# Optimization experiments

Hardware: AMD Instinct MI355X
Metric: run time of the kernel (lower is better)

Reference implementation:

```python
import jax, jax.numpy as jnp
import numpy as np

INPUT_DIM = 1024
NUM_OUTPUTS = 1024
BIT_SIZE = 256


def setup_inputs() -> dict:
    key = jax.random.key(0)
    k1, k2 = jax.random.split(key)
    # x: binary input bits, shape (input_dim, bit_size)
    x = jax.random.randint(k1, (INPUT_DIM, BIT_SIZE), 0, 2).astype(jnp.int32)
    # kernel: per-(input, output) Bernoulli probabilities in [0, 1)
    kernel = jax.random.uniform(k2, (INPUT_DIM, NUM_OUTPUTS), dtype=jnp.float32)
    return {"x": x, "kernel": kernel}


def reference(x, kernel):
    # Sample per-weight Bernoulli bit vectors: w[i, n, b] ~ Bernoulli(kernel[i, n])
    # (fused equivalent of the original nested-loop np.random.binomial calls)
    rng = jax.random.key(42)
    u = jax.random.uniform(rng, kernel.shape + (BIT_SIZE,), dtype=kernel.dtype)
    w = u < kernel[:, :, None]  # bool (input_dim, num_outputs, bit_size)

    # Original loop: temp = (x & w[:, n]).sum(axis=0); y[n] = (temp > 0)
    # == OR-reduction over input_dim of the bitwise AND.
    xb = x.astype(bool)  # (input_dim, bit_size)
    y = jnp.any(xb[:, None, :] & w, axis=0)  # (num_outputs, bit_size)
    return y.astype(jnp.float32)
```

## Files before the change

### kernel.cpp

```cpp
#include <hip/hip_runtime.h>


#define INPUT_DIM 1024
#define NUM_OUTPUTS 1024
#define BIT_SIZE 256

__device__ __forceinline__ uint32_t rotl32(uint32_t v, int r) {
    return (v << r) | (v >> (32 - r));
}

__device__ __forceinline__ void threefry2x32(uint32_t k0, uint32_t k1,
                                             uint32_t& x0, uint32_t& x1) {
    const uint32_t ks0 = k0;
    const uint32_t ks1 = k1;
    const uint32_t ks2 = k0 ^ k1 ^ 0x1BD11BDAu;
    x0 += ks0;
    x1 += ks1;
#define TF_ROUND(r) { x0 += x1; x1 = rotl32(x1, (r)); x1 ^= x0; }
    TF_ROUND(13) TF_ROUND(15) TF_ROUND(26) TF_ROUND(6)
    x0 += ks1; x1 += ks2 + 1u;
    TF_ROUND(17) TF_ROUND(29) TF_ROUND(16) TF_ROUND(24)
    x0 += ks2; x1 += ks0 + 2u;
    TF_ROUND(13) TF_ROUND(15) TF_ROUND(26) TF_ROUND(6)
    x0 += ks0; x1 += ks1 + 3u;
    TF_ROUND(17) TF_ROUND(29) TF_ROUND(16) TF_ROUND(24)
    x0 += ks1; x1 += ks2 + 4u;
    TF_ROUND(13) TF_ROUND(15) TF_ROUND(26) TF_ROUND(6)
    x0 += ks2; x1 += ks0 + 5u;
#undef TF_ROUND
}

__global__ __launch_bounds__(256) void BitLayer_25391846654323_kernel(
        const int* __restrict__ x,
        const float* __restrict__ kern,
        float* __restrict__ out) {
    const int tid = threadIdx.x;
    const int b = blockIdx.x >> 2;
    const int n = ((blockIdx.x & 3) << 8) + tid;
    const uint32_t nb = ((uint32_t)n << 8) | (uint32_t)b;
    const int wave = tid >> 6;
    const int lane = tid & 63;

    __shared__ uint32_t smask[32];
#pragma unroll
    for (int k = 0; k < 4; ++k) {
        const int i = (k << 8) + tid;
        const unsigned long long bal = __ballot(x[(i << 8) + b] != 0);
        if ((lane & 31) == 0) {
            smask[(k << 3) + (wave << 1) + (lane >> 5)] =
                (uint32_t)(bal >> (lane & 32));
        }
    }
    __syncthreads();

    uint32_t done = 0;
    for (int w = 0; w < 32; ++w) {
        uint32_t m = smask[w];
        while (m) {
            const int j = __builtin_ctz(m);
            m &= m - 1;
            const int i = (w << 5) + j;
            const float p = kern[(i << 10) + n];
            if (!done) {
                uint32_t c0 = (((uint32_t)(i & 511)) << 18) | nb;
                uint32_t c1 = c0 + (1u << 27);
                threefry2x32(0u, 42u, c0, c1);
                const uint32_t bits = (i < 512) ? c0 : c1;
                const float u = (float)(bits >> 9) * 0x1p-23f;
                if (u < p) done = 1u;
            }
            if (__all(done != 0)) goto finished;
        }
    }
finished:
    out[((uint32_t)n << 8) + (uint32_t)b] = done ? 1.0f : 0.0f;
}

extern "C" void kernel_launch(void* const* d_in, const int* in_sizes, int n_in,
                              void* d_out, int out_size, void* d_ws, size_t ws_size,
                              hipStream_t stream) {
    const int* x = (const int*)d_in[0];
    const float* kern = (const float*)d_in[1];
    float* out = (float*)d_out;

    BitLayer_25391846654323_kernel<<<NUM_OUTPUTS, 256, 0, stream>>>(x, kern, out);
}
```

Baseline: 66.48 us.

## Replace shared bitmask scan with batched, double-buffered prefetch of x and kernel

Drops the shared-memory ballot bitmask and barrier. Each thread now walks the input dimension in batches of 8, prefetching the next batch's x bits and kernel probabilities into registers while it computes the current batch. The goal is to hide global-load latency on the serial dependent loads. The cost is that the all-lanes-done early-exit check now runs only once per batch, and lanes that are already done still run the RNG inside a batch, so some extra threefry work and loads happen.

```diff
diff --git a/kernel.cpp b/kernel.cpp
--- a/kernel.cpp
+++ b/kernel.cpp
@@ -4,6 +4,7 @@
 #define INPUT_DIM 1024
 #define NUM_OUTPUTS 1024
 #define BIT_SIZE 256
+#define BATCH 8
 
 __device__ __forceinline__ uint32_t rotl32(uint32_t v, int r) {
     return (v << r) | (v >> (32 - r));
@@ -38,41 +39,45 @@
     const int b = blockIdx.x >> 2;
     const int n = ((blockIdx.x & 3) << 8) + tid;
     const uint32_t nb = ((uint32_t)n << 8) | (uint32_t)b;
-    const int wave = tid >> 6;
-    const int lane = tid & 63;
-
-    __shared__ uint32_t smask[32];
-#pragma unroll
-    for (int k = 0; k < 4; ++k) {
-        const int i = (k << 8) + tid;
-        const unsigned long long bal = __ballot(x[(i << 8) + b] != 0);
-        if ((lane & 31) == 0) {
-            smask[(k << 3) + (wave << 1) + (lane >> 5)] =
-                (uint32_t)(bal >> (lane & 32));
-        }
-    }
-    __syncthreads();
 
     uint32_t done = 0;
-    for (int w = 0; w < 32; ++w) {
-        uint32_t m = smask[w];
-        while (m) {
-            const int j = __builtin_ctz(m);
-            m &= m - 1;
-            const int i = (w << 5) + j;
-            const float p = kern[(i << 10) + n];
-            if (!done) {
+
+    int xb[BATCH];
+    float p[BATCH];
+#pragma unroll
+    for (int k = 0; k < BATCH; ++k) {
+        xb[k] = x[(k << 8) + b];
+        p[k] = kern[(k << 10) + n];
+    }
+
+    for (int i0 = 0; i0 < INPUT_DIM; i0 += BATCH) {
+        const int i1 = (i0 + BATCH) & (INPUT_DIM - 1);
+        int xb2[BATCH];
+        float p2[BATCH];
+#pragma unroll
+        for (int k = 0; k < BATCH; ++k) {
+            xb2[k] = x[((i1 + k) << 8) + b];
+            p2[k] = kern[((i1 + k) << 10) + n];
+        }
+
+#pragma unroll
+        for (int k = 0; k < BATCH; ++k) {
+            if (xb[k] != 0) {
+                const int i = i0 + k;
                 uint32_t c0 = (((uint32_t)(i & 511)) << 18) | nb;
                 uint32_t c1 = c0 + (1u << 27);
                 threefry2x32(0u, 42u, c0, c1);
                 const uint32_t bits = (i < 512) ? c0 : c1;
                 const float u = (float)(bits >> 9) * 0x1p-23f;
-                if (u < p) done = 1u;
+                if (u < p[k]) done = 1u;
             }
-            if (__all(done != 0)) goto finished;
         }
+        if (__all(done != 0)) break;
+
+#pragma unroll
+        for (int k = 0; k < BATCH; ++k) { xb[k] = xb2[k]; p[k] = p2[k]; }
     }
-finished:
+
     out[((uint32_t)n << 8) + (uint32_t)b] = done ? 1.0f : 0.0f;
 }
 
```

Measured after the change: 62.79 us. 1.06x faster.
